# Optimization experiments

Measured on AMD Instinct MI355X. Metric: run time of the kernel, lower is better.

The kernel has to match this reference:

```python
import jax, jax.numpy as jnp
import numpy as np
from jax import lax

# ---- model/config constants (from EVL.__init__ with voxel_meters = 0.1) ----
B, C_IN, G = 2, 64, 64          # batch, neck_final channels, voxel grid side
HID = 128                        # head_hidden_dim
NUM_CLASS = 34                   # efm3d taxonomy size
BBOX_MIN, BBOX_MAX = 0.1, 6.0
VOXEL_M = 0.1
OFFSET_MAX = 2.0 * VOXEL_M       # self.offset_max
YAW_MAX = 1.6
DET_THRESH = 0.2
SPLAT_SIGMA = max(1, int(0.12 / VOXEL_M))   # = 1
NMS_RADIUS = SPLAT_SIGMA + 1                 # = 2
TOP_K = 128
VE = (-3.2, 3.2, -3.2, 3.2, -3.2, 3.2)       # xmin,xmax,ymin,ymax,zmin,zmax


def conv3d(x, w, b):
    # x: [B,Ci,D,H,W], w: [Co,Ci,kd,kh,kw]
    y = lax.conv_general_dilated(x, w, (1, 1, 1), 'SAME',
                                 dimension_numbers=('NCDHW', 'OIDHW', 'NCDHW'))
    return y + b[None, :, None, None, None]


def head(x, w1, b1, w2, b2, wf, bf):
    # VolumeCNNHead: two 3x3x3 conv+ReLU layers then 1x1x1 projection
    x = jax.nn.relu(conv3d(x, w1, b1))
    x = jax.nn.relu(conv3d(x, w2, b2))
    return conv3d(x, wf, bf)


def maxpool3d(x, r):
    k = 2 * r + 1
    return lax.reduce_window(x, -jnp.inf, lax.max,
                             (1, 1, k, k, k), (1, 1, 1, 1, 1), 'SAME')


def simple_nms3d(scores, nms_radius):
    # SuperPoint-style iterative windowed NMS, 3D.
    zeros = jnp.zeros_like(scores)
    max_mask = scores == maxpool3d(scores, nms_radius)
    for _ in range(2):
        supp = maxpool3d(max_mask.astype(scores.dtype), nms_radius) > 0
        supp_scores = jnp.where(supp, zeros, scores)
        new_max = supp_scores == maxpool3d(supp_scores, nms_radius)
        max_mask = max_mask | (new_max & ~supp)
    return jnp.where(max_mask, scores, zeros)


def voxel2obb(cent_nms, bbox, clas, ve, top_k, thresh):
    # cent_nms: [B,1,D,H,W], bbox: [B,7,D,H,W], clas: [B,C,D,H,W]
    b, _, D, H, W = cent_nms.shape
    flat = cent_nms.reshape(b, -1)
    scores, idx = lax.top_k(flat, top_k)                  # [B,K]
    iz = idx // (H * W)
    iy = (idx // W) % H
    ix = idx % W
    vx = (ve[1] - ve[0]) / W
    vy = (ve[3] - ve[2]) / H
    vz = (ve[5] - ve[4]) / D
    cx = ve[0] + (ix.astype(jnp.float32) + 0.5) * vx
    cy = ve[2] + (iy.astype(jnp.float32) + 0.5) * vy
    cz = ve[4] + (iz.astype(jnp.float32) + 0.5) * vz
    vox_center = jnp.stack([cx, cy, cz], axis=-1)          # [B,K,3]
    bb = jnp.take_along_axis(bbox.reshape(b, 7, -1), idx[:, None, :], axis=2)  # [B,7,K]
    bb = jnp.transpose(bb, (0, 2, 1))                      # [B,K,7]
    sizes = bb[..., 0:3]
    center = vox_center + bb[..., 3:6]
    yaw = bb[..., 6:7]
    valid = (scores > thresh).astype(scores.dtype)         # [B,K]
    dets = jnp.concatenate([center, sizes, yaw,
                            scores[..., None], valid[..., None]], axis=-1)  # [B,K,9]
    dets = dets * valid[..., None]  # emulate threshold filtering with padding
    cp = jnp.take_along_axis(clas.reshape(b, clas.shape[1], -1),
                             idx[:, None, :], axis=2)      # [B,C,K]
    cp = jnp.transpose(cp, (0, 2, 1)) * valid[..., None]   # [B,K,C]
    return jnp.concatenate([dets, cp], axis=-1)            # [B,K,9+C]


def setup_inputs() -> dict:
    key = jax.random.key(0)
    ks = jax.random.split(key, 16)
    inp = {'neck_feats': jax.random.normal(ks[0], (B, C_IN, G, G, G), jnp.float32)}
    i = 1
    for name, fdim, fbias in [('cent', 1, -5.0), ('bbox', 7, 0.0), ('clas', NUM_CLASS, 0.0)]:
        inp[f'{name}_w1'] = jax.random.normal(ks[i], (HID, C_IN, 3, 3, 3), jnp.float32) / np.float32(np.sqrt(C_IN * 27)); i += 1
        inp[f'{name}_b1'] = jnp.zeros((HID,), jnp.float32)
        inp[f'{name}_w2'] = jax.random.normal(ks[i], (HID, HID, 3, 3, 3), jnp.float32) / np.float32(np.sqrt(HID * 27)); i += 1
        inp[f'{name}_b2'] = jnp.zeros((HID,), jnp.float32)
        inp[f'{name}_wf'] = jax.random.normal(ks[i], (fdim, HID, 1, 1, 1), jnp.float32) / np.float32(np.sqrt(HID)); i += 1
        inp[f'{name}_bf'] = jnp.full((fdim,), fbias, jnp.float32)
    return inp


def reference(neck_feats,
              cent_w1, cent_b1, cent_w2, cent_b2, cent_wf, cent_bf,
              bbox_w1, bbox_b1, bbox_w2, bbox_b2, bbox_wf, bbox_bf,
              clas_w1, clas_b1, clas_w2, clas_b2, clas_wf, clas_bf):
    # heads
    cent_pr = jax.nn.sigmoid(head(neck_feats, cent_w1, cent_b1, cent_w2, cent_b2, cent_wf, cent_bf))
    bbox_raw = head(neck_feats, bbox_w1, bbox_b1, bbox_w2, bbox_b2, bbox_wf, bbox_bf)
    # bbox decode: sizes in [bbox_min, bbox_max], offsets in [-offset_max, offset_max], yaw in [-yaw_max, yaw_max]
    sizes = (BBOX_MAX - BBOX_MIN) * jax.nn.sigmoid(bbox_raw[:, 0:3]) + BBOX_MIN
    offs = OFFSET_MAX * jnp.tanh(bbox_raw[:, 3:6])
    yaw = YAW_MAX * jnp.tanh(bbox_raw[:, 6:7])
    bbox_pr = jnp.concatenate([sizes, offs, yaw], axis=1)   # [B,7,D,H,W]
    clas_pr = jax.nn.softmax(head(neck_feats, clas_w1, clas_b1, clas_w2, clas_b2, clas_wf, clas_bf), axis=1)
    # post_process
    cent_nms = simple_nms3d(cent_pr, NMS_RADIUS)
    dets = voxel2obb(cent_nms, bbox_pr, clas_pr, VE, TOP_K, DET_THRESH)
    return dets  # [B, 128, 9 + NUM_CLASS]
```

## Files before the change

kernel.cpp:

```cpp
#include <hip/hip_runtime.h>
#include <math.h>

#define Gd 64
#define G2 4096
#define G3 262144
#define CIN 64
#define HIDC 128
#define NB 2
#define TOPKN 128
#define NCLASS 34
#define CAPN 65536
#define DET_TH 0.2f

#define NBDATA ((size_t)4096*66*64)
#define PLANEB ((size_t)64*66*128)
#define H1SZ   ((size_t)66*PLANEB)
#define ZPAGEB 16384
#define ASCALE 16.0f

typedef unsigned char u8;
typedef unsigned short u16;
typedef unsigned int u32;
typedef unsigned long long u64;
typedef int i32x4  __attribute__((ext_vector_type(4)));
typedef int i32x16 __attribute__((ext_vector_type(16)));

__device__ __forceinline__ void glds16(const void* g, void* l){
    __builtin_amdgcn_global_load_lds(
        (const __attribute__((address_space(1))) void*)g,
        (__attribute__((address_space(3))) void*)l, 16, 0, 0);
}

__global__ void wmax_k(const float* __restrict__ w, int n, u32* __restrict__ slot){
    float m = 0.f;
    for (int i = blockIdx.x*256 + threadIdx.x; i < n; i += gridDim.x*256)
        m = fmaxf(m, fabsf(w[i]));
    #pragma unroll
    for (int off=32; off>0; off>>=1)
        m = fmaxf(m, __shfl_xor(m, off));
    if ((threadIdx.x & 63) == 0)
        atomicMax(slot, __float_as_uint(m));
}

__global__ void repack1b_k(const float* __restrict__ w, u8* __restrict__ wq, const u32* __restrict__ slot){
    int i = blockIdx.x*256 + threadIdx.x;
    if (i >= 27*128*64) return;
    float sw = __uint_as_float(*slot) / 127.f;
    int tap = i >> 13;
    int r   = i & 8191;
    int co  = r >> 6;
    int ci  = r & 63;
    float v = w[((size_t)co*64 + ci)*27 + tap];
    int q = (int)rintf(v / sw);
    q = q < -127 ? -127 : (q > 127 ? 127 : q);
    int chunk = ci >> 5, gg = (ci>>4)&1, e = ci&15;
    size_t dst = (((size_t)(tap*2 + chunk)*256 + gg*128 + co))*16 + e;
    wq[dst] = (u8)(signed char)q;
}

__global__ void repack2_k(const float* __restrict__ w, u8* __restrict__ wq, const u32* __restrict__ slot){
    int i = blockIdx.x*256 + threadIdx.x;
    if (i >= 27*128*128) return;
    float sw = __uint_as_float(*slot) / 127.f;
    int tap = i >> 14;
    int r   = i & 16383;
    int co  = r >> 7;
    int ci  = r & 127;
    float v = w[((size_t)co*128 + ci)*27 + tap];
    int q = (int)rintf(v / sw);
    q = q < -127 ? -127 : (q > 127 ? 127 : q);
    int chunk = ci >> 5, gg = (ci>>4)&1, e = ci&15;
    size_t dst = (((size_t)(tap*4 + chunk)*256 + gg*128 + co))*16 + e;
    wq[dst] = (u8)(signed char)q;
}

__global__ void init_k(int* cnt, u32* slots, u8* zpage){
    int t = threadIdx.x;
    if (t < NB) cnt[t]=0;
    if (t < 2)  slots[t]=0;
    for (int e=t; e<ZPAGEB; e+=256) zpage[e]=0;
}

__global__ void zero_planes_k(u8* __restrict__ h1q, size_t h1stride, int nreg){
    const int perplane = (int)(PLANEB/16);
    int i = blockIdx.x*256 + threadIdx.x;
    int reg = i / (2*perplane);
    if (reg >= nreg) return;
    int r = i - reg*2*perplane;
    size_t off = (size_t)reg*h1stride
               + ((r < perplane) ? (size_t)r*16
                                 : (size_t)65*PLANEB + (size_t)(r-perplane)*16);
    uint4 z; z.x=z.y=z.z=z.w=0u;
    *(uint4*)(h1q + off) = z;
}

__global__ void __launch_bounds__(256) nbconv_k(const float* __restrict__ in,
                                                u8* __restrict__ nbq, size_t nbstride){
    const int blk = blockIdx.x;
    const int batch = blk >> 12;
    const int zy = blk & 4095;
    const int t  = threadIdx.x;
    __shared__ u8 sh[64][64];
    const int x = t & 63, wv = t >> 6;
    const float* src = in + (size_t)batch*CIN*G3 + (size_t)zy*64;
    u8* dst = nbq + (size_t)batch*nbstride;
    #pragma unroll
    for (int r=0;r<16;++r){
        int ci = wv*16 + r;
        float a = src[(size_t)ci*G3 + x];
        int q = (int)rintf(a * ASCALE);
        q = q < -127 ? -127 : (q > 127 ? 127 : q);
        sh[x][ci] = (u8)(signed char)q;
    }
    __syncthreads();
    const size_t obase = (size_t)zy*66*64;
    {
        int xx = t >> 2, part = t & 3;
        *(uint4*)(dst + obase + (size_t)(xx+1)*64 + part*16) = *(const uint4*)&sh[xx][part*16];
    }
    if (t < 32){
        int px = (t<16)?0:65; int off = (t&15)*4;
        *(u32*)(dst + obase + (size_t)px*64 + off) = 0u;
    }
}

#define ACT_U 3168
#define WG_U  1792

__device__ __forceinline__ void xcd_decode2(int b, int& yt, int& zt){
    int xcd = b & 7, j = b >> 3;
    yt = xcd*2 + (j & 1);
    zt = j >> 1;
}

#define LOADTAP(TAP_, TL_, WV, AV) { \
    int dz_=(TAP_)/9, r9_=(TAP_)-dz_*9, dy_=r9_/3, dx_=r9_-dy_*3; \
    const int wb_ = (TL_)*256 + g*128 + n; \
    _Pragma("unroll") \
    for (int mt_=0; mt_<4; ++mt_) WV[mt_] = wlds[wb_ + mt_*32]; \
    int rowb_ = ((sz+dz_)*6 + (sy+dy_))*66; \
    _Pragma("unroll") \
    for (int j_=0;j_<2;++j_){ \
        int xpos_ = j_*32 + n + dx_; \
        AV[j_] = acth[(rowb_ + xpos_)*2 + (g ^ ((xpos_>>2)&1))]; } }

#define MFMA8(WV, AV) { \
    _Pragma("unroll") \
    for (int j_=0;j_<2;++j_){ \
        i32x4 av_ = *(const i32x4*)&AV[j_]; \
        _Pragma("unroll") \
        for (int mt_=0;mt_<4;++mt_){ \
            i32x4 wv_ = *(const i32x4*)&WV[mt_]; \
            acc[mt_][j_] = __builtin_amdgcn_mfma_i32_32x32x32_i8(wv_, av_, acc[mt_][j_],0,0,0); } } }

#define TAPGROUP(TS_, TC_) { \
    uint4 wvA[4], avA[2], wvB[4], avB[2]; \
    LOADTAP(TS_, 0, wvA, avA); \
    _Pragma("unroll") \
    for (int tl=0; tl<(TC_); ++tl){ \
        if (tl & 1){ \
            if (tl+1 < (TC_)) LOADTAP((TS_)+tl+1, tl+1, wvA, avA); \
            MFMA8(wvB, avB); \
        } else { \
            if (tl+1 < (TC_)) LOADTAP((TS_)+tl+1, tl+1, wvB, avB); \
            MFMA8(wvA, avA); \
        } \
    } }

__global__ void __launch_bounds__(512,2) conv1_mfma(
    const u8* __restrict__ nbq, const u8* __restrict__ zpage,
    const u8* __restrict__ wq,
    const float* __restrict__ b1, const u32* __restrict__ slot,
    u8* __restrict__ h1q, size_t nbstride, size_t h1stride)
{
    const int blk = blockIdx.x;
    const int batch = blk >> 9;
    int yt, zt; xcd_decode2(blk & 511, yt, zt);
    const int t  = threadIdx.x;
    const int lane = t & 63;
    const int w  = t >> 6;
    const int sz = w >> 2;
    const int sy = w & 3;
    const int n  = lane & 31;
    const int g  = lane >> 5;

    __shared__ uint4 lds[ACT_U + WG_U];
    uint4* acth = lds;
    uint4* wlds = lds + ACT_U;

    const u8* nbb = nbq + (size_t)batch*nbstride;
    u8* h1b = h1q + (size_t)batch*h1stride;
    const float dq1 = (__uint_as_float(*slot) / 127.f) * (1.0f/ASCALE);
    const int pblk = 1 + 2*zt;

    if (t < 96){
        int row = t>>2, rem = t&3;
        int x = (rem&1)?65:0, s = rem>>1;
        uint4 z; z.x=z.y=z.z=z.w=0u;
        acth[(row*66+x)*2 + s] = z;
    }

    const u8* srcA[6]; int dstA[6];
    #pragma unroll
    for (int p=0;p<6;++p){
        int u = t + p*512;
        int row = u>>7, r = u&127;
        int x = 1 + (r>>1), s = r&1;
        int gg = s ^ ((x>>2)&1);
        int zr = row/6, yr = row - zr*6;
        int zin = pblk - 2 + zr;
        int y   = 4*yt - 1 + yr;
        const u8* a = zpage;
        if ((unsigned)y < 64u && (unsigned)zin < 64u)
            a = nbb + (((size_t)zin*64 + y)*66 + x)*64 + gg*16;
        srcA[p] = a;
        int ub = (t & ~63) + p*512;
        dstA[p] = ub + 4*(ub>>7) + 2;
    }
    const int wq4 = w & 3;
    const int wk0 = w >> 2;

    i32x16 acc[4][2];
    #pragma unroll
    for (int a=0;a<4;++a)
        #pragma unroll
        for (int b2_=0;b2_<2;++b2_)
            #pragma unroll
            for (int r=0;r<16;++r) acc[a][b2_][r]=0;

    for (int c=0; c<2; ++c){
        #pragma unroll
        for (int p=0;p<6;++p)
            glds16(srcA[p] + c*32, &acth[dstA[p]]);
        int ts = 0;
        #pragma unroll
        for (int grp=0; grp<4; ++grp){
            const int tc = (grp<3)?7:6;
            for (int k=wk0; k<tc; k+=2)
                glds16(wq + (((size_t)(ts+k)*2 + c)*256 + wq4*64 + lane)*16,
                       &wlds[k*256 + wq4*64]);
            __syncthreads();
            __builtin_amdgcn_s_setprio(1);
            TAPGROUP(ts, tc)
            __builtin_amdgcn_s_setprio(0);
            __syncthreads();
            ts += tc;
        }
    }

    u32* ols = (u32*)lds;
    if (t < 256){
        int row = t>>5, xsel = (t>>4)&1, c4 = (t&15)*2;
        int pos = row*66 + (xsel?65:0);
        ols[pos*33 + c4] = 0u;
        ols[pos*33 + c4 + 1] = 0u;
    }
    #pragma unroll
    for (int mt=0;mt<4;++mt){
        float bvals[16];
        #pragma unroll
        for (int r=0;r<16;++r)
            bvals[r] = b1[mt*32 + (r&3) + 8*(r>>2) + 4*g];
        #pragma unroll
        for (int j=0;j<2;++j){
            int pos = w*66 + j*32 + n + 1;
            #pragma unroll
            for (int q=0;q<4;++q){
                u32 packed = 0;
                #pragma unroll
                for (int i=0;i<4;++i){
                    int r = q*4 + i;
                    float v = (float)acc[mt][j][r] * dq1 + bvals[r];
                    v = v>0.f ? v : 0.f;
                    int qv = (int)rintf(v * ASCALE);
                    qv = qv > 127 ? 127 : qv;
                    packed |= ((u32)(u8)qv) << (8*i);
                }
                ols[pos*33 + mt*8 + g + 2*q] = packed;
            }
        }
    }
    __syncthreads();
    for (int k=t; k<4224; k+=512){
        int pos = k>>3, q = k&7;
        int row = pos/66, x = pos - row*66;
        int base = pos*33 + q*4;
        uint4 v;
        v.x = ols[base+0]; v.y = ols[base+1]; v.z = ols[base+2]; v.w = ols[base+3];
        int p_  = pblk + (row>>2);
        int yo_ = 4*yt + (row&3);
        *(uint4*)(h1b + (((size_t)p_*64 + yo_)*66 + x)*128 + q*16) = v;
    }
}

__global__ void __launch_bounds__(512,2) conv2_mfma(
    const u8* __restrict__ h1q, const u8* __restrict__ zpage,
    const u8* __restrict__ wq,
    const float* __restrict__ b2, const float* __restrict__ wf,
    const float* __restrict__ bf, const u32* __restrict__ slot,
    float* __restrict__ scores, size_t h1stride)
{
    const int blk = blockIdx.x;
    const int batch = blk >> 9;
    int yt, zt; xcd_decode2(blk & 511, yt, zt);
    const int t  = threadIdx.x;
    const int lane = t & 63;
    const int w  = t >> 6;
    const int sz = w >> 2;
    const int sy = w & 3;
    const int n  = lane & 31;
    const int g  = lane >> 5;

    __shared__ uint4 lds[ACT_U + WG_U];
    uint4* acth = lds;
    uint4* wlds = lds + ACT_U;

    const u8* h1b = h1q + (size_t)batch*h1stride;
    const float dq2 = (__uint_as_float(*slot) / 127.f) * (1.0f/ASCALE);

    if (t < 96){
        int row = t>>2, rem = t&3;
        int x = (rem&1)?65:0, s = rem>>1;
        uint4 z; z.x=z.y=z.z=z.w=0u;
        acth[(row*66+x)*2 + s] = z;
    }

    const u8* srcA[6]; int dstA[6];
    #pragma unroll
    for (int p=0;p<6;++p){
        int u = t + p*512;
        int row = u>>7, r = u&127;
        int x = 1 + (r>>1), s = r&1;
        int gg = s ^ ((x>>2)&1);
        int zr = row/6, yr = row - zr*6;
        int pp = 2*zt + zr;
        int y  = 4*yt - 1 + yr;
        const u8* a = zpage;
        if ((unsigned)y < 64u)
            a = h1b + (((size_t)pp*64 + y)*66 + x)*128 + gg*16;
        srcA[p] = a;
        int ub = (t & ~63) + p*512;
        dstA[p] = ub + 4*(ub>>7) + 2;
    }
    const int wq4 = w & 3;
    const int wk0 = w >> 2;

    i32x16 acc[4][2];
    #pragma unroll
    for (int a=0;a<4;++a)
        #pragma unroll
        for (int b2_=0;b2_<2;++b2_)
            #pragma unroll
            for (int r=0;r<16;++r) acc[a][b2_][r]=0;

    for (int c=0; c<4; ++c){
        #pragma unroll
        for (int p=0;p<6;++p)
            glds16(srcA[p] + c*32, &acth[dstA[p]]);
        int ts = 0;
        #pragma unroll
        for (int grp=0; grp<4; ++grp){
            const int tc = (grp<3)?7:6;
            for (int k=wk0; k<tc; k+=2)
                glds16(wq + (((size_t)(ts+k)*4 + c)*256 + wq4*64 + lane)*16,
                       &wlds[k*256 + wq4*64]);
            __syncthreads();
            __builtin_amdgcn_s_setprio(1);
            TAPGROUP(ts, tc)
            __builtin_amdgcn_s_setprio(0);
            __syncthreads();
            ts += tc;
        }
    }

    float part[2] = {0.f, 0.f};
    #pragma unroll
    for (int mt=0;mt<4;++mt){
        #pragma unroll
        for (int r=0;r<16;++r){
            int co = mt*32 + (r&3) + 8*(r>>2) + 4*g;
            float b2v = b2[co], wfv = wf[co];
            #pragma unroll
            for (int j=0;j<2;++j){
                float v = (float)acc[mt][j][r] * dq2 + b2v;
                v = v>0.f?v:0.f;
                part[j] = fmaf(v, wfv, part[j]);
            }
        }
    }
    const int z = 2*zt + sz;
    const int yo = 4*yt + sy;
    float bfv = bf[0];
    float* scb = scores + (size_t)batch*G3;
    #pragma unroll
    for (int j=0;j<2;++j){
        float tot = part[j] + __shfl_xor(part[j], 32);
        if (g==0)
            scb[((size_t)z*64 + yo)*64 + j*32 + n] = 1.f/(1.f+expf(-(tot+bfv)));
    }
}

__global__ void __launch_bounds__(256) pool_xy_k(const float* __restrict__ in, float* __restrict__ out){
    const int plane = blockIdx.x;
    __shared__ float sp[64][65];
    const float* src = in + (size_t)plane*G2;
    const int t = threadIdx.x;
    for (int e=t; e<4096; e+=256){
        int y=e>>6, x=e&63;
        float v = src[e];
        if (x>=1)  v=fmaxf(v, src[e-1]);
        if (x>=2)  v=fmaxf(v, src[e-2]);
        if (x<=62) v=fmaxf(v, src[e+1]);
        if (x<=61) v=fmaxf(v, src[e+2]);
        sp[y][x]=v;
    }
    __syncthreads();
    float* dst = out + (size_t)plane*G2;
    for (int e=t; e<4096; e+=256){
        int y=e>>6, x=e&63;
        float v = sp[y][x];
        if (y>=1)  v=fmaxf(v, sp[y-1][x]);
        if (y>=2)  v=fmaxf(v, sp[y-2][x]);
        if (y<=62) v=fmaxf(v, sp[y+1][x]);
        if (y<=61) v=fmaxf(v, sp[y+2][x]);
        dst[e]=v;
    }
}

__device__ __forceinline__ float zpool5(const float* __restrict__ a, int i){
    int p = (i >> 12) & 63;
    float v = a[i];
    if (p >= 1)  v = fmaxf(v, a[i - 4096]);
    if (p >= 2)  v = fmaxf(v, a[i - 8192]);
    if (p <= 62) v = fmaxf(v, a[i + 4096]);
    if (p <= 61) v = fmaxf(v, a[i + 8192]);
    return v;
}

__global__ void poolz_eq_k(const float* __restrict__ tA, const float* __restrict__ scores,
                           float* __restrict__ mask){
    int i = blockIdx.x*256 + threadIdx.x;
    if (i >= NB*G3) return;
    mask[i] = (scores[i] == zpool5(tA, i)) ? 1.f : 0.f;
}
__global__ void poolz_supp_k(const float* __restrict__ tA, const float* __restrict__ scores,
                             float* __restrict__ supp, float* __restrict__ ss){
    int i = blockIdx.x*256 + threadIdx.x;
    if (i >= NB*G3) return;
    bool sp = zpool5(tA, i) > 0.f;
    supp[i] = sp ? 1.f : 0.f;
    ss[i]   = sp ? 0.f : scores[i];
}
__global__ void poolz_upd_k(const float* __restrict__ tA, const float* __restrict__ ss,
                            const float* __restrict__ supp, float* __restrict__ mask){
    int i = blockIdx.x*256 + threadIdx.x;
    if (i >= NB*G3) return;
    bool nm = (ss[i] == zpool5(tA, i)) && (supp[i] == 0.f);
    mask[i] = (mask[i] != 0.f || nm) ? 1.f : 0.f;
}

__global__ void compact_k(const float* __restrict__ mask, const float* __restrict__ s,
                          float* __restrict__ lv, int* __restrict__ li, int* __restrict__ cnt){
    int i = blockIdx.x*256 + threadIdx.x;
    if (i >= NB*G3) return;
    if (mask[i]!=0.f && s[i] > DET_TH){
        int b = i >> 18;
        int pos = atomicAdd(&cnt[b],1);
        if (pos < CAPN){
            lv[(size_t)b*CAPN+pos] = s[i];
            li[(size_t)b*CAPN+pos] = i & (G3-1);
        }
    }
}

__device__ __forceinline__ void bitonic2048_desc(u64* sk, int t){
    for (int k=2; k<=2048; k<<=1){
        for (int j=k>>1; j>0; j>>=1){
            #pragma unroll 4
            for (int i=t; i<2048; i+=256){
                int x = i ^ j;
                if (x > i){
                    bool dirDesc = ((i & k) == 0);
                    u64 a = sk[i], b = sk[x];
                    bool sw = dirDesc ? (a < b) : (a > b);
                    if (sw){ sk[i]=b; sk[x]=a; }
                }
            }
            __syncthreads();
        }
    }
}

__global__ void __launch_bounds__(256) topsort_k(const float* __restrict__ lv, const int* __restrict__ li,
                        const int* __restrict__ cnt, float* __restrict__ tv, int* __restrict__ ti){
    const int b = blockIdx.x;
    const int t = threadIdx.x;
    __shared__ u64 sk[2048];
    int n = cnt[b]; if (n > CAPN) n = CAPN;
    const float* Lv = lv + (size_t)b*CAPN;
    const int*   Li = li + (size_t)b*CAPN;

    for (int e=t; e<2048; e+=256){
        u64 key = 0ull;
        if (e < n)
            key = ((u64)__float_as_uint(Lv[e])<<32) | (u32)(~Li[e]);
        sk[e] = key;
    }
    int processed = n < 2048 ? n : 2048;
    __syncthreads();
    bitonic2048_desc(sk, t);
    while (processed < n){
        int chunk = n - processed; if (chunk > 1920) chunk = 1920;
        for (int e=t; e<1920; e+=256){
            u64 key = 0ull;
            if (e < chunk)
                key = ((u64)__float_as_uint(Lv[processed+e])<<32) | (u32)(~Li[processed+e]);
            sk[128+e] = key;
        }
        processed += chunk;
        __syncthreads();
        bitonic2048_desc(sk, t);
    }
    if (t < TOPKN){
        u64 key = sk[t];
        if (key){
            tv[b*TOPKN+t] = __uint_as_float((u32)(key>>32));
            ti[b*TOPKN+t] = (int)(~(u32)key);
        } else {
            tv[b*TOPKN+t] = 0.f;
            ti[b*TOPKN+t] = 0;
        }
    }
}

__global__ void __launch_bounds__(512) perdet_k(
    const float* __restrict__ neck,
    const float* __restrict__ tv, const int* __restrict__ ti,
    const float* __restrict__ bw1, const float* __restrict__ bb1,
    const float* __restrict__ bw2, const float* __restrict__ bb2,
    const float* __restrict__ bwf, const float* __restrict__ bbf,
    const float* __restrict__ lw1, const float* __restrict__ lb1,
    const float* __restrict__ lw2, const float* __restrict__ lb2,
    const float* __restrict__ lwf, const float* __restrict__ lbf,
    float* __restrict__ out)
{
    const int blk = blockIdx.x;
    const int b = blk >> 7, r = blk & 127;
    const int t = threadIdx.x;
    float score = tv[b*TOPKN + r];
    int   idx   = ti[b*TOPKN + r];
    float* orow = out + ((size_t)b*TOPKN + r)*43;
    if (!(score > DET_TH)){
        if (t < 43) orow[t] = 0.f;
        return;
    }
    const int iz = idx >> 12, iy = (idx>>6)&63, ix = idx&63;

    __shared__ float pin[CIN][125];
    __shared__ float h1s[27][HIDC];
    __shared__ float h2s[HIDC];
    __shared__ float raws[7+NCLASS];

    const float* inb = neck + (size_t)b*CIN*G3;
    for (int e=t; e<CIN*125; e+=512){
        int ci=e/125, q=e-ci*125;
        int pz=q/25, py=(q/5)%5, px=q%5;
        int gz=iz-2+pz, gy=iy-2+py, gx=ix-2+px;
        float v=0.f;
        if ((unsigned)gz<64u && (unsigned)gy<64u && (unsigned)gx<64u)
            v = inb[(size_t)ci*G3 + (size_t)gz*G2 + gy*Gd + gx];
        pin[ci][q]=v;
    }
    __syncthreads();

    for (int head=0; head<2; ++head){
        const float* w1 = head? lw1 : bw1;
        const float* b1 = head? lb1 : bb1;
        const float* w2 = head? lw2 : bw2;
        const float* b2 = head? lb2 : bb2;
        const float* wf = head? lwf : bwf;
        const float* bf = head? lbf : bbf;
        const int fdim  = head? NCLASS : 7;

        for (int e=t; e<27*HIDC; e+=512){
            int co = e & 127, pos = e >> 7;
            int pdz=pos/9, pdy=(pos/3)%3, pdx=pos%3;
            int gz=iz-1+pdz, gy=iy-1+pdy, gx=ix-1+pdx;
            float acc = 0.f;
            if ((unsigned)gz<64u && (unsigned)gy<64u && (unsigned)gx<64u){
                acc = b1[co];
                const float* wco = w1 + (size_t)co*CIN*27;
                for (int ci=0; ci<CIN; ++ci){
                    const float* pr = pin[ci];
                    const float* wr = wco + ci*27;
                    #pragma unroll
                    for (int tz=0;tz<3;++tz)
                        #pragma unroll
                        for (int ty=0;ty<3;++ty)
                            #pragma unroll
                            for (int tx=0;tx<3;++tx)
                                acc = fmaf(pr[(pdz+tz)*25+(pdy+ty)*5+(pdx+tx)],
                                           wr[(tz*3+ty)*3+tx], acc);
                }
                acc = acc>0.f ? acc : 0.f;
            }
            h1s[pos][co]=acc;
        }
        __syncthreads();

        if (t < HIDC){
            float acc = b2[t];
            const float* wco = w2 + (size_t)t*HIDC*27;
            for (int pos=0; pos<27; ++pos){
                const float* hr = h1s[pos];
                for (int ci=0; ci<HIDC; ++ci)
                    acc = fmaf(hr[ci], wco[ci*27+pos], acc);
            }
            h2s[t] = acc>0.f ? acc : 0.f;
        }
        __syncthreads();

        if (t < fdim){
            float acc = bf[t];
            const float* wr = wf + t*HIDC;
            for (int ci=0; ci<HIDC; ++ci) acc = fmaf(h2s[ci], wr[ci], acc);
            raws[(head?7:0)+t] = acc;
        }
        __syncthreads();
    }

    if (t==0){
        const float vx = (float)(6.4/64.0);
        float cx = -3.2f + ((float)ix + 0.5f)*vx;
        float cy = -3.2f + ((float)iy + 0.5f)*vx;
        float cz = -3.2f + ((float)iz + 0.5f)*vx;
        float sx = 5.9f*(1.f/(1.f+expf(-raws[0]))) + 0.1f;
        float sy = 5.9f*(1.f/(1.f+expf(-raws[1]))) + 0.1f;
        float sz = 5.9f*(1.f/(1.f+expf(-raws[2]))) + 0.1f;
        float ox = 0.2f*tanhf(raws[3]);
        float oy = 0.2f*tanhf(raws[4]);
        float oz = 0.2f*tanhf(raws[5]);
        float yw = 1.6f*tanhf(raws[6]);
        orow[0]=cx+ox; orow[1]=cy+oy; orow[2]=cz+oz;
        orow[3]=sx; orow[4]=sy; orow[5]=sz;
        orow[6]=yw; orow[7]=score; orow[8]=1.f;
        float mx = raws[7];
        #pragma unroll
        for (int i=1;i<NCLASS;++i) mx = fmaxf(mx, raws[7+i]);
        float ev[NCLASS]; float sum=0.f;
        #pragma unroll
        for (int i=0;i<NCLASS;++i){ ev[i]=expf(raws[7+i]-mx); sum+=ev[i]; }
        float inv = 1.f/sum;
        #pragma unroll
        for (int i=0;i<NCLASS;++i) orow[9+i] = ev[i]*inv;
    }
}

extern "C" void kernel_launch(void* const* d_in, const int* in_sizes, int n_in,
                              void* d_out, int out_size, void* d_ws, size_t ws_size,
                              hipStream_t stream)
{
    (void)in_sizes; (void)n_in; (void)out_size;
    const float* neck = (const float*)d_in[0];
    const float* ce_w1=(const float*)d_in[1],  *ce_b1=(const float*)d_in[2];
    const float* ce_w2=(const float*)d_in[3],  *ce_b2=(const float*)d_in[4];
    const float* ce_wf=(const float*)d_in[5],  *ce_bf=(const float*)d_in[6];
    const float* bb_w1=(const float*)d_in[7],  *bb_b1=(const float*)d_in[8];
    const float* bb_w2=(const float*)d_in[9],  *bb_b2=(const float*)d_in[10];
    const float* bb_wf=(const float*)d_in[11], *bb_bf=(const float*)d_in[12];
    const float* cl_w1=(const float*)d_in[13], *cl_b1=(const float*)d_in[14];
    const float* cl_w2=(const float*)d_in[15], *cl_b2=(const float*)d_in[16];
    const float* cl_wf=(const float*)d_in[17], *cl_bf=(const float*)d_in[18];
    float* out = (float*)d_out;
    char* ws = (char*)d_ws;

    float* scores=(float*)(ws + 0);
    float* tA    =(float*)(ws + (2u<<20));
    float* mask  =(float*)(ws + (8u<<20));
    float* supp  =(float*)(ws + (10u<<20));
    float* ssb   =(float*)(ws + (12u<<20));
    float* lv    =(float*)(ws + (14u<<20));
    int*   li    =(int*)  (ws + (14u<<20) + (512u<<10));
    float* tv    =(float*)(ws + (15u<<20));
    int*   ti    =(int*)  (ws + (15u<<20) + 4096);
    int*   cnt   =(int*)  (ws + (15u<<20) + 8192);
    u32*   slots =(u32*)  (ws + (15u<<20) + 12288);
    u8*    wq1   =(u8*)   (ws + (15u<<20) + 16384);
    u8*    wq2   =(u8*)   (ws + (16u<<20));
    u8*    zpage =(u8*)   (ws + (17u<<20));
    u8*    nbq   =(u8*)   (ws + (18u<<20));
    const size_t need_fast = (53u<<20) + 2*H1SZ;
    const bool fast = (ws_size >= need_fast);
    u8* h1q = (u8*)(ws + (fast ? (53u<<20) : (36u<<20)));

    init_k<<<1, 256, 0, stream>>>(cnt, slots, zpage);
    wmax_k<<<256, 256, 0, stream>>>(ce_w1, 27*128*64,  &slots[0]);
    wmax_k<<<256, 256, 0, stream>>>(ce_w2, 27*128*128, &slots[1]);
    repack1b_k<<<(27*128*64 +255)/256, 256, 0, stream>>>(ce_w1, wq1, &slots[0]);
    repack2_k<<<(27*128*128+255)/256, 256, 0, stream>>>(ce_w2, wq2, &slots[1]);

    const int ppl = (int)(PLANEB/16);
    if (fast){
        zero_planes_k<<<(2*2*ppl+255)/256, 256, 0, stream>>>(h1q, H1SZ, 2);
        nbconv_k<<<NB*4096, 256, 0, stream>>>(neck, nbq, NBDATA);
        conv1_mfma<<<NB*512, 512, 0, stream>>>(nbq, zpage, wq1, ce_b1, &slots[0],
                                               h1q, NBDATA, H1SZ);
        conv2_mfma<<<NB*512, 512, 0, stream>>>(h1q, zpage, wq2, ce_b2, ce_wf, ce_bf,
                                               &slots[1], scores, H1SZ);
    } else {
        zero_planes_k<<<(2*ppl+255)/256, 256, 0, stream>>>(h1q, 0, 1);
        for (int b=0; b<NB; ++b){
            nbconv_k<<<4096, 256, 0, stream>>>(neck + (size_t)b*CIN*G3, nbq, 0);
            conv1_mfma<<<512, 512, 0, stream>>>(nbq, zpage, wq1, ce_b1, &slots[0],
                                                h1q, 0, 0);
            conv2_mfma<<<512, 512, 0, stream>>>(h1q, zpage, wq2, ce_b2, ce_wf, ce_bf,
                                                &slots[1], scores + (size_t)b*G3, 0);
        }
    }

    const int n = NB*G3, nb = n/256;
    pool_xy_k<<<NB*64,256,0,stream>>>(scores, tA);
    poolz_eq_k<<<nb,256,0,stream>>>(tA, scores, mask);
    for (int it=0; it<2; ++it){
        pool_xy_k<<<NB*64,256,0,stream>>>(mask, tA);
        poolz_supp_k<<<nb,256,0,stream>>>(tA, scores, supp, ssb);
        pool_xy_k<<<NB*64,256,0,stream>>>(ssb, tA);
        poolz_upd_k<<<nb,256,0,stream>>>(tA, ssb, supp, mask);
    }

    compact_k<<<nb,256,0,stream>>>(mask, scores, lv, li, cnt);
    topsort_k<<<NB,256,0,stream>>>(lv, li, cnt, tv, ti);
    perdet_k<<<NB*TOPKN,512,0,stream>>>(neck, tv, ti,
        bb_w1,bb_b1,bb_w2,bb_b2,bb_wf,bb_bf,
        cl_w1,cl_b1,cl_w2,cl_b2,cl_wf,cl_bf, out);
}
```

Baseline: 501.2 us.

## Fuse separable NMS pooling into tiled 3D kernel and stagger conv tap order

Replaces the two-kernel (xy-plane then z-stencil) max-pool passes with a single tiled 3D pooling kernel. It loads a 20^3 halo tile into LDS, does separable x/y/z max in shared memory and applies the mask/suppress/update logic in the same pass, which removes the tA intermediate round trips and halves the NMS launch count. Separately, each wave in the conv kernels starts its tap loop at a different rotation to spread LDS bank/weight access contention. The pool kernel uses only 128 blocks with about 57KB of LDS each, which may limit parallelism, and the tap rotation turns the tap index into a runtime value.

```diff
diff --git a/kernel.cpp b/kernel.cpp
--- a/kernel.cpp
+++ b/kernel.cpp
@@ -154,15 +154,17 @@
             acc[mt_][j_] = __builtin_amdgcn_mfma_i32_32x32x32_i8(wv_, av_, acc[mt_][j_],0,0,0); } } }
 
 #define TAPGROUP(TS_, TC_) { \
+    int rot_ = wrot_; if (rot_ >= (TC_)) rot_ -= (TC_); \
     uint4 wvA[4], avA[2], wvB[4], avB[2]; \
-    LOADTAP(TS_, 0, wvA, avA); \
+    LOADTAP((TS_)+rot_, rot_, wvA, avA); \
     _Pragma("unroll") \
     for (int tl=0; tl<(TC_); ++tl){ \
+        int rn_ = rot_ + tl + 1; if (rn_ >= (TC_)) rn_ -= (TC_); \
         if (tl & 1){ \
-            if (tl+1 < (TC_)) LOADTAP((TS_)+tl+1, tl+1, wvA, avA); \
+            if (tl+1 < (TC_)) LOADTAP((TS_)+rn_, rn_, wvA, avA); \
             MFMA8(wvB, avB); \
         } else { \
-            if (tl+1 < (TC_)) LOADTAP((TS_)+tl+1, tl+1, wvB, avB); \
+            if (tl+1 < (TC_)) LOADTAP((TS_)+rn_, rn_, wvB, avB); \
             MFMA8(wvA, avA); \
         } \
     } }
@@ -183,6 +185,7 @@
     const int sy = w & 3;
     const int n  = lane & 31;
     const int g  = lane >> 5;
+    const int wrot_ = w;
 
     __shared__ uint4 lds[ACT_U + WG_U];
     uint4* acth = lds;
@@ -310,6 +313,7 @@
     const int sy = w & 3;
     const int n  = lane & 31;
     const int g  = lane >> 5;
+    const int wrot_ = w;
 
     __shared__ uint4 lds[ACT_U + WG_U];
     uint4* acth = lds;
@@ -400,63 +404,68 @@
     }
 }
 
-__global__ void __launch_bounds__(256) pool_xy_k(const float* __restrict__ in, float* __restrict__ out){
-    const int plane = blockIdx.x;
-    __shared__ float sp[64][65];
-    const float* src = in + (size_t)plane*G2;
+__global__ void __launch_bounds__(256) pool3d_k(
+    const float* __restrict__ in, const float* __restrict__ scores,
+    float* __restrict__ supp, float* __restrict__ outA, int mode)
+{
+    __shared__ float a[8000];
+    __shared__ float b[6400];
+    const int blk = blockIdx.x;
+    const int batch = blk >> 6;
+    const int rem = blk & 63;
+    const int tz = rem >> 4, ty = (rem >> 2) & 3, tx = rem & 3;
+    const int z0 = tz*16, y0 = ty*16, x0 = tx*16;
     const int t = threadIdx.x;
+    const float* inb = in + (size_t)batch*G3;
+
+    for (int e=t; e<8000; e+=256){
+        int zz = e/400, r2 = e-zz*400;
+        int yy = r2/20, xx = r2-yy*20;
+        int gz = z0-2+zz, gy = y0-2+yy, gx = x0-2+xx;
+        float v = -3.4e38f;
+        if ((unsigned)gz<64u && (unsigned)gy<64u && (unsigned)gx<64u)
+            v = inb[(size_t)gz*G2 + gy*64 + gx];
+        a[e] = v;
+    }
+    __syncthreads();
+    for (int e=t; e<6400; e+=256){
+        int zz = e/320, r2 = e-zz*320;
+        int yy = r2>>4, xx = r2&15;
+        int base = zz*400 + yy*20 + xx;
+        float m = a[base];
+        m = fmaxf(m, a[base+1]); m = fmaxf(m, a[base+2]);
+        m = fmaxf(m, a[base+3]); m = fmaxf(m, a[base+4]);
+        b[e] = m;
+    }
+    __syncthreads();
+    for (int e=t; e<5120; e+=256){
+        int zz = e/256, r2 = e&255;
+        int yy = r2>>4, xx = r2&15;
+        int base = zz*320 + yy*16 + xx;
+        float m = b[base];
+        m = fmaxf(m, b[base+16]); m = fmaxf(m, b[base+32]);
+        m = fmaxf(m, b[base+48]); m = fmaxf(m, b[base+64]);
+        a[e] = m;
+    }
+    __syncthreads();
     for (int e=t; e<4096; e+=256){
-        int y=e>>6, x=e&63;
-        float v = src[e];
-        if (x>=1)  v=fmaxf(v, src[e-1]);
-        if (x>=2)  v=fmaxf(v, src[e-2]);
-        if (x<=62) v=fmaxf(v, src[e+1]);
-        if (x<=61) v=fmaxf(v, src[e+2]);
-        sp[y][x]=v;
-    }
-    __syncthreads();
-    float* dst = out + (size_t)plane*G2;
-    for (int e=t; e<4096; e+=256){
-        int y=e>>6, x=e&63;
-        float v = sp[y][x];
-        if (y>=1)  v=fmaxf(v, sp[y-1][x]);
-        if (y>=2)  v=fmaxf(v, sp[y-2][x]);
-        if (y<=62) v=fmaxf(v, sp[y+1][x]);
-        if (y<=61) v=fmaxf(v, sp[y+2][x]);
-        dst[e]=v;
-    }
-}
-
-__device__ __forceinline__ float zpool5(const float* __restrict__ a, int i){
-    int p = (i >> 12) & 63;
-    float v = a[i];
-    if (p >= 1)  v = fmaxf(v, a[i - 4096]);
-    if (p >= 2)  v = fmaxf(v, a[i - 8192]);
-    if (p <= 62) v = fmaxf(v, a[i + 4096]);
-    if (p <= 61) v = fmaxf(v, a[i + 8192]);
-    return v;
-}
-
-__global__ void poolz_eq_k(const float* __restrict__ tA, const float* __restrict__ scores,
-                           float* __restrict__ mask){
-    int i = blockIdx.x*256 + threadIdx.x;
-    if (i >= NB*G3) return;
-    mask[i] = (scores[i] == zpool5(tA, i)) ? 1.f : 0.f;
-}
-__global__ void poolz_supp_k(const float* __restrict__ tA, const float* __restrict__ scores,
-                             float* __restrict__ supp, float* __restrict__ ss){
-    int i = blockIdx.x*256 + threadIdx.x;
-    if (i >= NB*G3) return;
-    bool sp = zpool5(tA, i) > 0.f;
-    supp[i] = sp ? 1.f : 0.f;
-    ss[i]   = sp ? 0.f : scores[i];
-}
-__global__ void poolz_upd_k(const float* __restrict__ tA, const float* __restrict__ ss,
-                            const float* __restrict__ supp, float* __restrict__ mask){
-    int i = blockIdx.x*256 + threadIdx.x;
-    if (i >= NB*G3) return;
-    bool nm = (ss[i] == zpool5(tA, i)) && (supp[i] == 0.f);
-    mask[i] = (mask[i] != 0.f || nm) ? 1.f : 0.f;
+        int zz = e>>8, yy = (e>>4)&15, xx = e&15;
+        int base = zz*256 + yy*16 + xx;
+        float m = a[base];
+        m = fmaxf(m, a[base+256]); m = fmaxf(m, a[base+512]);
+        m = fmaxf(m, a[base+768]); m = fmaxf(m, a[base+1024]);
+        size_t i = (size_t)batch*G3 + (size_t)(z0+zz)*G2 + (y0+yy)*64 + (x0+xx);
+        if (mode == 0){
+            outA[i] = (m == in[i]) ? 1.f : 0.f;
+        } else if (mode == 1){
+            bool sp = m > 0.f;
+            supp[i] = sp ? 1.f : 0.f;
+            outA[i] = sp ? 0.f : scores[i];
+        } else {
+            bool nm = (m == in[i]) && (supp[i] == 0.f);
+            outA[i] = (outA[i] != 0.f || nm) ? 1.f : 0.f;
+        }
+    }
 }
 
 __global__ void compact_k(const float* __restrict__ mask, const float* __restrict__ s,
@@ -675,7 +684,6 @@
     char* ws = (char*)d_ws;
 
     float* scores=(float*)(ws + 0);
-    float* tA    =(float*)(ws + (2u<<20));
     float* mask  =(float*)(ws + (8u<<20));
     float* supp  =(float*)(ws + (10u<<20));
     float* ssb   =(float*)(ws + (12u<<20));
@@ -718,16 +726,13 @@
         }
     }
 
-    const int n = NB*G3, nb = n/256;
-    pool_xy_k<<<NB*64,256,0,stream>>>(scores, tA);
-    poolz_eq_k<<<nb,256,0,stream>>>(tA, scores, mask);
+    pool3d_k<<<NB*64,256,0,stream>>>(scores, scores, supp, mask, 0);
     for (int it=0; it<2; ++it){
-        pool_xy_k<<<NB*64,256,0,stream>>>(mask, tA);
-        poolz_supp_k<<<nb,256,0,stream>>>(tA, scores, supp, ssb);
-        pool_xy_k<<<NB*64,256,0,stream>>>(ssb, tA);
-        poolz_upd_k<<<nb,256,0,stream>>>(tA, ssb, supp, mask);
-    }
-
+        pool3d_k<<<NB*64,256,0,stream>>>(mask, scores, supp, ssb, 1);
+        pool3d_k<<<NB*64,256,0,stream>>>(ssb, scores, supp, mask, 2);
+    }
+
+    const int nb = NB*G3/256;
     compact_k<<<nb,256,0,stream>>>(mask, scores, lv, li, cnt);
     topsort_k<<<NB,256,0,stream>>>(lv, li, cnt, tv, ti);
     perdet_k<<<NB*TOPKN,512,0,stream>>>(neck, tv, ti,
```

New measurement: 534.5 us, median of 2. 6.6% more time.
